# Kernel optimization log

Hardware: AMD Instinct MI355X
Metric: run time of the kernel (lower is better)

## Reference

```python
import jax, jax.numpy as jnp
import numpy as np

V = 65536      # vocab_size_v
H = 512        # hidden_size
M = 16         # max word length (m)
N = 8192       # number of words in the ragged batch
IH = H // 4    # char embedding dim / LSTM input size
HH = H // 2    # LSTM hidden size per direction


def setup_inputs() -> dict:
    key = jax.random.key(0)
    ks = jax.random.split(key, 16)
    word_ids = jax.random.randint(ks[0], (N,), 0, V, dtype=jnp.int32)
    is_oov = jax.random.randint(ks[1], (N,), 0, 2, dtype=jnp.int32)
    char_ids = jax.random.randint(ks[2], (N, M), 0, 256, dtype=jnp.int32)
    char_lens = jax.random.randint(ks[3], (N,), 1, M + 1, dtype=jnp.int32)
    lstm_scale = 1.0 / np.sqrt(HH)
    return {
        "word_ids": word_ids,
        "is_oov": is_oov,
        "char_ids": char_ids,
        "char_lens": char_lens,
        "word_emb": jax.random.normal(ks[4], (V, H), jnp.float32) * 0.02,
        "char_emb": jax.random.normal(ks[5], (256, IH), jnp.float32) * 0.02,
        "w_ih_f": jax.random.uniform(ks[6], (4 * HH, IH), jnp.float32, -lstm_scale, lstm_scale),
        "w_hh_f": jax.random.uniform(ks[7], (4 * HH, HH), jnp.float32, -lstm_scale, lstm_scale),
        "b_ih_f": jax.random.uniform(ks[8], (4 * HH,), jnp.float32, -lstm_scale, lstm_scale),
        "b_hh_f": jax.random.uniform(ks[9], (4 * HH,), jnp.float32, -lstm_scale, lstm_scale),
        "w_ih_b": jax.random.uniform(ks[10], (4 * HH, IH), jnp.float32, -lstm_scale, lstm_scale),
        "w_hh_b": jax.random.uniform(ks[11], (4 * HH, HH), jnp.float32, -lstm_scale, lstm_scale),
        "b_ih_b": jax.random.uniform(ks[12], (4 * HH,), jnp.float32, -lstm_scale, lstm_scale),
        "b_hh_b": jax.random.uniform(ks[13], (4 * HH,), jnp.float32, -lstm_scale, lstm_scale),
        "proj_w": jax.random.normal(ks[14], (H, H), jnp.float32) * 0.02,
        "proj_b": jax.random.normal(ks[15], (H,), jnp.float32) * 0.02,
    }


def _lstm_final_hidden(x, lens, w_ih, w_hh, b_ih, b_hh):
    """Batched variable-length LSTM; returns final hidden state h_T per sequence.

    x: [N, M, IH], lens: [N]. Carry is frozen once t >= len (emulating per-word
    batch-size-1 LSTM calls on unpadded sequences). PyTorch gate order i,f,g,o.
    """
    n = x.shape[0]
    gx = jnp.einsum("nmi,gi->nmg", x, w_ih) + b_ih + b_hh        # [N, M, 4HH]
    mask = (jnp.arange(M)[None, :] < lens[:, None])[..., None]    # [N, M, 1]

    def step(carry, inp):
        h, c = carry
        g_t, m_t = inp                                            # [N,4HH], [N,1]
        g = g_t + h @ w_hh.T
        i, f, gg, o = jnp.split(g, 4, axis=-1)
        i = jax.nn.sigmoid(i)
        f = jax.nn.sigmoid(f)
        gg = jnp.tanh(gg)
        o = jax.nn.sigmoid(o)
        c_new = f * c + i * gg
        h_new = o * jnp.tanh(c_new)
        h = jnp.where(m_t, h_new, h)
        c = jnp.where(m_t, c_new, c)
        return (h, c), None

    h0 = jnp.zeros((n, HH), x.dtype)
    c0 = jnp.zeros((n, HH), x.dtype)
    (h, _), _ = jax.lax.scan(step, (h0, c0),
                             (gx.transpose(1, 0, 2), mask.transpose(1, 0, 2)))
    return h  # [N, HH]


def reference(word_ids, is_oov, char_ids, char_lens,
              word_emb, char_emb,
              w_ih_f, w_hh_f, b_ih_f, b_hh_f,
              w_ih_b, w_hh_b, b_ih_b, b_hh_b,
              proj_w, proj_b):
    # Char-level path (computed for all words, selected only where OOV).
    x = char_emb[char_ids]                                        # [N, M, IH]
    h_fwd = _lstm_final_hidden(x, char_lens, w_ih_f, w_hh_f, b_ih_f, b_hh_f)
    # Backward direction: reverse each sequence within its true length.
    rev_idx = jnp.clip(char_lens[:, None] - 1 - jnp.arange(M)[None, :], 0, M - 1)
    x_rev = jnp.take_along_axis(x, rev_idx[..., None], axis=1)    # [N, M, IH]
    h_bwd = _lstm_final_hidden(x_rev, char_lens, w_ih_b, w_hh_b, b_ih_b, b_hh_b)
    char_word_embed = jnp.concatenate([h_fwd, h_bwd], axis=-1)    # [N, H]

    vocab_embed = word_emb[word_ids]                              # [N, H]
    sel = jnp.where(is_oov[:, None] > 0, char_word_embed, vocab_embed)
    return sel @ proj_w.T + proj_b                                # [N, H]
```

## Files before the change

kernel.cpp:

```cpp
#include <hip/hip_runtime.h>
#include <math.h>

#define VOCAB   65536
#define HDIM    512
#define MLEN    16
#define NWORDS  8192
#define IHDIM   128
#define HHDIM   256

#define TMW 32
#define TP  32

#define B_WHH 0u
#define B_GX2 1048576u
#define B_PBF 5242880u
#define B_PBB 5767168u
#define B_CHE 5769216u
#define B_INT 14157824u

typedef _Float16 f16x8 __attribute__((ext_vector_type(8)));
typedef float    f32x4 __attribute__((ext_vector_type(4)));
union U4H8 { uint4 u; f16x8 h; _Float16 e[8]; };

__device__ __forceinline__ unsigned packh2(float lo, float hi) {
    union { _Float16 h[2]; unsigned u; } v;
    v.h[0] = (_Float16)lo; v.h[1] = (_Float16)hi;
    return v.u;
}

__device__ __forceinline__ float sigf(float x)  { return 1.0f / (1.0f + __expf(-x)); }
__device__ __forceinline__ float tanh_f(float x){ return 1.0f - 2.0f / (__expf(2.0f * x) + 1.0f); }

__device__ __forceinline__ void load_lds_128(const void* g, void* l) {
    __builtin_amdgcn_global_load_lds((const __attribute__((address_space(1))) unsigned*)g,
                                     (__attribute__((address_space(3))) unsigned*)l, 16, 0, 0);
}

__global__ void prep_k(const float* __restrict__ whhf, const float* __restrict__ whhb,
                       const float* __restrict__ projw, const float* __restrict__ projb,
                       char* __restrict__ wsb) {
    int i = blockIdx.x * blockDim.x + threadIdx.x;
    if (i < 65536) {
        int dir = i >> 15, r = i & 32767, kt = r >> 12, r2 = r & 4095, ntg = r2 >> 6, lane = r2 & 63;
        const float* whh = dir ? whhb : whhf;
        int n  = ntg * 16 + (lane & 15);
        int k0 = kt * 32 + (lane >> 4) * 8;
        unsigned q[4];
        #pragma unroll
        for (int jj = 0; jj < 4; ++jj)
            q[jj] = packh2(whh[n * HHDIM + k0 + 2 * jj], whh[n * HHDIM + k0 + 2 * jj + 1]);
        ((uint4*)(wsb + B_WHH))[i] = make_uint4(q[0], q[1], q[2], q[3]);
    }
    if (i < 32768) {
        int kt = i >> 11, r = i & 2047, nt = r >> 6, lane = r & 63;
        int j  = nt * 16 + (lane & 15);
        int k0 = kt * 32 + (lane >> 4) * 8;
        unsigned q[4];
        #pragma unroll
        for (int jj = 0; jj < 4; ++jj)
            q[jj] = packh2(projw[j * HDIM + k0 + 2 * jj], projw[j * HDIM + k0 + 2 * jj + 1]);
        ((uint4*)(wsb + B_PBF))[i] = make_uint4(q[0], q[1], q[2], q[3]);
    }
    if (i < 512) ((float*)(wsb + B_PBB))[i] = projb[i];
}

__global__ void gxc_k(const float* __restrict__ wihf, const float* __restrict__ wihb,
                      const float* __restrict__ bihf, const float* __restrict__ bhhf,
                      const float* __restrict__ bihb, const float* __restrict__ bhhb,
                      const float* __restrict__ chemb, char* __restrict__ wsb) {
    const int dir = blockIdx.x >> 8, cid = blockIdx.x & 255;
    __shared__ __align__(16) float emb[IHDIM];
    __shared__ float gxl[1024];
    if (threadIdx.x < IHDIM) emb[threadIdx.x] = chemb[cid * IHDIM + threadIdx.x];
    __syncthreads();
    const float* wih = dir ? wihb : wihf;
    const float* bih = dir ? bihb : bihf;
    const float* bhh = dir ? bhhb : bhhf;
    #pragma unroll
    for (int p = 0; p < 4; ++p) {
        int n = threadIdx.x + p * 256;
        float acc = bih[n] + bhh[n];
        const float4* w4 = (const float4*)(wih + n * IHDIM);
        const float4* e4 = (const float4*)emb;
        #pragma unroll 8
        for (int k4 = 0; k4 < 32; ++k4) {
            float4 w = w4[k4], e = e4[k4];
            acc = fmaf(w.x, e.x, fmaf(w.y, e.y, fmaf(w.z, e.z, fmaf(w.w, e.w, acc))));
        }
        gxl[n] = acc;
    }
    __syncthreads();
    uint4* outp = (uint4*)(wsb + B_GX2) + (size_t)(dir * 256 + cid) * 512;
    #pragma unroll
    for (int s = 0; s < 2; ++s) {
        int tid2 = threadIdx.x + s * 256;
        int wv = tid2 >> 6, col = tid2 & 15;
        U4H8 v;
        #pragma unroll
        for (int g = 0; g < 4; ++g)
            #pragma unroll
            for (int c = 0; c < 2; ++c)
                v.e[g * 2 + c] = (_Float16)gxl[g * 256 + wv * 32 + c * 16 + col];
        outp[tid2] = v.u;
    }
}

__global__ void count_k(const int* __restrict__ is_oov, const int* __restrict__ lens,
                        int* __restrict__ ip) {
    int n = blockIdx.x * blockDim.x + threadIdx.x;
    if (n < NWORDS && is_oov[n] > 0) atomicAdd(&ip[lens[n] - 1], 1);
}

__global__ void prefix_k(int* __restrict__ ip) {
    if (threadIdx.x == 0) {
        int total = 0;
        for (int b = 15; b >= 0; --b) { ip[16 + b] = total; ip[32 + b] = total; total += ip[b]; }
        ip[48] = total;
    }
}

__global__ void scatter_k(const int* __restrict__ is_oov, const int* __restrict__ lens,
                          int* __restrict__ ip) {
    int n = blockIdx.x * blockDim.x + threadIdx.x;
    if (n < NWORDS && is_oov[n] > 0) {
        int pos = atomicAdd(&ip[32 + lens[n] - 1], 1);
        ip[64 + pos] = n;
    }
}

__global__ __launch_bounds__(512, 2)
void lstm_k(const int* __restrict__ char_ids, const int* __restrict__ lens,
            const char* __restrict__ wsb, const int* __restrict__ ip) {
    const int dir = blockIdx.y;
    const int tid = threadIdx.x;
    const int total = ip[48];
    const int w0 = blockIdx.x * TMW;
    if (w0 >= total) return;
    const int wcount = min(TMW, total - w0);
    const int* sorted = ip + 64;

    __shared__ int n_s[TMW], len_s[TMW];
    __shared__ int cid_s[MLEN][TMW];
    __shared__ __align__(16) _Float16 Zh[TMW][264];
    __shared__ __align__(16) uint4 wbuf[8][2][512];

    if (tid < TMW) {
        int idx = w0 + min(tid, wcount - 1);
        n_s[tid] = sorted[idx];
        len_s[tid] = (tid < wcount) ? lens[sorted[idx]] : 0;
    }
    for (int i = tid; i < TMW * 132; i += 512) ((unsigned*)Zh)[i] = 0u;
    __syncthreads();
    {
        int m = tid >> 4, t = tid & 15;
        int L = len_s[m];
        int pos = dir ? max(L - 1 - t, 0) : t;
        cid_s[t][m] = char_ids[n_s[m] * MLEN + pos];
    }

    const int wv = tid >> 6, lane = tid & 63, col = lane & 15, quad = lane >> 4;
    int lenr[2][4];
    #pragma unroll
    for (int mt = 0; mt < 2; ++mt)
        #pragma unroll
        for (int r = 0; r < 4; ++r) lenr[mt][r] = len_s[mt * 16 + quad * 4 + r];
    const int maxlen = len_s[0];

    const uint4* wpg = (const uint4*)(wsb + B_WHH) + (size_t)dir * 32768;
    const uint4* gx2 = (const uint4*)(wsb + B_GX2) + (size_t)dir * 131072;

    float cst[2][2][4];
    #pragma unroll
    for (int c = 0; c < 2; ++c)
        #pragma unroll
        for (int mt = 0; mt < 2; ++mt)
            #pragma unroll
            for (int r = 0; r < 4; ++r) cst[c][mt][r] = 0.0f;

    auto stage = [&](int kt, int buf) {
        #pragma unroll
        for (int gc = 0; gc < 8; ++gc) {
            int ntg = (gc >> 1) * 16 + wv * 2 + (gc & 1);
            load_lds_128(wpg + (kt * 4096 + ntg * 64 + lane), &wbuf[wv][buf][gc * 64]);
        }
    };
    stage(0, 0);
    __syncthreads();

    for (int t = 0; t < maxlen; ++t) {
        U4H8 gq[2][4];
        #pragma unroll
        for (int mt = 0; mt < 2; ++mt)
            #pragma unroll
            for (int r = 0; r < 4; ++r)
                gq[mt][r].u = gx2[(size_t)cid_s[t][mt * 16 + quad * 4 + r] * 512 + tid];

        f32x4 acc[4][2][2];
        #pragma unroll
        for (int g = 0; g < 4; ++g)
            #pragma unroll
            for (int c = 0; c < 2; ++c)
                #pragma unroll
                for (int mt = 0; mt < 2; ++mt) {
                    f32x4 a;
                    #pragma unroll
                    for (int r = 0; r < 4; ++r) a[r] = (float)gq[mt][r].e[g * 2 + c];
                    acc[g][c][mt] = a;
                }

        #pragma unroll
        for (int kt = 0; kt < 8; ++kt) {
            const int buf = kt & 1;
            stage((kt + 1) & 7, buf ^ 1);
            __builtin_amdgcn_s_waitcnt(0x0F78);
            f16x8 af0 = *(const f16x8*)&Zh[col][kt * 32 + quad * 8];
            f16x8 af1 = *(const f16x8*)&Zh[16 + col][kt * 32 + quad * 8];
            #pragma unroll
            for (int g = 0; g < 4; ++g)
                #pragma unroll
                for (int c = 0; c < 2; ++c) {
                    U4H8 b; b.u = wbuf[wv][buf][(g * 2 + c) * 64 + lane];
                    acc[g][c][0] = __builtin_amdgcn_mfma_f32_16x16x32_f16(af0, b.h, acc[g][c][0], 0, 0, 0);
                    acc[g][c][1] = __builtin_amdgcn_mfma_f32_16x16x32_f16(af1, b.h, acc[g][c][1], 0, 0, 0);
                }
        }
        __syncthreads();

        #pragma unroll
        for (int mt = 0; mt < 2; ++mt)
            #pragma unroll
            for (int r = 0; r < 4; ++r) {
                if (t < lenr[mt][r]) {
                    const int m = mt * 16 + quad * 4 + r;
                    #pragma unroll
                    for (int c = 0; c < 2; ++c) {
                        float i_ = sigf(acc[0][c][mt][r]);
                        float f_ = sigf(acc[1][c][mt][r]);
                        float g_ = tanh_f(acc[2][c][mt][r]);
                        float o_ = sigf(acc[3][c][mt][r]);
                        float cn = f_ * cst[c][mt][r] + i_ * g_;
                        cst[c][mt][r] = cn;
                        Zh[m][wv * 32 + c * 16 + col] = (_Float16)(o_ * tanh_f(cn));
                    }
                }
            }
        __syncthreads();
    }

    unsigned short* cheh = (unsigned short*)(wsb + B_CHE);
    for (int i = tid; i < TMW * HHDIM; i += 512) {
        int m = i >> 8, u = i & 255;
        if (m < wcount) {
            union { _Float16 h; unsigned short s; } v; v.h = Zh[m][u];
            __builtin_nontemporal_store(v.s, cheh + (size_t)n_s[m] * HDIM + dir * HHDIM + u);
        }
    }
}

__global__ __launch_bounds__(512, 2)
void proj_k(const int* __restrict__ word_ids, const int* __restrict__ is_oov,
            const float* __restrict__ word_emb, const char* __restrict__ wsb,
            float* __restrict__ out) {
    const int tid = threadIdx.x;
    const int n0 = blockIdx.x * TP;
    __shared__ __align__(16) _Float16 Zp[TP][520];

    for (int f = tid; f < TP * 128; f += 512) {
        int w = f >> 7, s4 = f & 127;
        int n = n0 + w;
        if (is_oov[n] > 0) {
            ushort4 hv = ((const ushort4*)((const unsigned short*)(wsb + B_CHE) + (size_t)n * HDIM))[s4];
            *(ushort4*)&Zp[w][s4 * 4] = hv;
        } else {
            float4 v = ((const float4*)(word_emb + (size_t)word_ids[n] * HDIM))[s4];
            Zp[w][s4 * 4 + 0] = (_Float16)v.x;
            Zp[w][s4 * 4 + 1] = (_Float16)v.y;
            Zp[w][s4 * 4 + 2] = (_Float16)v.z;
            Zp[w][s4 * 4 + 3] = (_Float16)v.w;
        }
    }
    __syncthreads();

    const int wv = tid >> 6, lane = tid & 63, col = lane & 15, quad = lane >> 4;
    const float* pbb = (const float*)(wsb + B_PBB);
    f32x4 acc[4][2];
    #pragma unroll
    for (int c = 0; c < 4; ++c) {
        float b = pbb[wv * 64 + c * 16 + col];
        acc[c][0] = (f32x4){b, b, b, b};
        acc[c][1] = (f32x4){b, b, b, b};
    }

    const uint4* pbf = (const uint4*)(wsb + B_PBF);
    #pragma unroll
    for (int kt = 0; kt < 16; ++kt) {
        f16x8 af0 = *(const f16x8*)&Zp[col][kt * 32 + quad * 8];
        f16x8 af1 = *(const f16x8*)&Zp[16 + col][kt * 32 + quad * 8];
        #pragma unroll
        for (int c = 0; c < 4; ++c) {
            U4H8 b; b.u = pbf[(size_t)kt * 2048 + (wv * 4 + c) * 64 + lane];
            acc[c][0] = __builtin_amdgcn_mfma_f32_16x16x32_f16(af0, b.h, acc[c][0], 0, 0, 0);
            acc[c][1] = __builtin_amdgcn_mfma_f32_16x16x32_f16(af1, b.h, acc[c][1], 0, 0, 0);
        }
    }

    #pragma unroll
    for (int mt = 0; mt < 2; ++mt)
        #pragma unroll
        for (int r = 0; r < 4; ++r) {
            const size_t m = n0 + mt * 16 + quad * 4 + r;
            #pragma unroll
            for (int c = 0; c < 4; ++c)
                __builtin_nontemporal_store(acc[c][mt][r], &out[m * HDIM + wv * 64 + c * 16 + col]);
        }
}

extern "C" void kernel_launch(void* const* d_in, const int* in_sizes, int n_in,
                              void* d_out, int out_size, void* d_ws, size_t ws_size,
                              hipStream_t stream) {
    const int*   word_ids  = (const int*)d_in[0];
    const int*   is_oov    = (const int*)d_in[1];
    const int*   char_ids  = (const int*)d_in[2];
    const int*   char_lens = (const int*)d_in[3];
    const float* word_emb  = (const float*)d_in[4];
    const float* char_emb  = (const float*)d_in[5];
    const float* w_ih_f    = (const float*)d_in[6];
    const float* w_hh_f    = (const float*)d_in[7];
    const float* b_ih_f    = (const float*)d_in[8];
    const float* b_hh_f    = (const float*)d_in[9];
    const float* w_ih_b    = (const float*)d_in[10];
    const float* w_hh_b    = (const float*)d_in[11];
    const float* b_ih_b    = (const float*)d_in[12];
    const float* b_hh_b    = (const float*)d_in[13];
    const float* proj_w    = (const float*)d_in[14];
    const float* proj_b    = (const float*)d_in[15];
    float* out = (float*)d_out;
    char*  wsb = (char*)d_ws;
    int*   ip  = (int*)(wsb + B_INT);

    hipMemsetAsync(ip, 0, 256, stream);
    prep_k<<<256, 256, 0, stream>>>(w_hh_f, w_hh_b, proj_w, proj_b, wsb);
    gxc_k<<<512, 256, 0, stream>>>(w_ih_f, w_ih_b, b_ih_f, b_hh_f, b_ih_b, b_hh_b, char_emb, wsb);
    count_k<<<NWORDS / 256, 256, 0, stream>>>(is_oov, char_lens, ip);
    prefix_k<<<1, 64, 0, stream>>>(ip);
    scatter_k<<<NWORDS / 256, 256, 0, stream>>>(is_oov, char_lens, ip);
    lstm_k<<<dim3(NWORDS / TMW, 2), 512, 0, stream>>>(char_ids, char_lens, wsb, ip);
    proj_k<<<NWORDS / TP, 512, 0, stream>>>(word_ids, is_oov, word_emb, wsb, out);
}
```

Baseline: 474.3 us.

## Keep part of W_hh in registers, restructure gx precompute, enlarge proj tile

The gate-input precompute is split into a kernel that stages W_ih rows in shared memory and writes an fp32 intermediate, plus a separate fp16 pack kernel. In the LSTM kernel, the first three k-tiles of W_hh are held in registers across all timesteps, so only the remaining tiles are streamed into LDS each step with a different waitcnt schedule. The LSTM grid is flattened so forward and backward blocks interleave, and the projection tile grows to 64 words per block for more reuse of the projection weights. These changes add register pressure, an extra launch and an extra intermediate buffer.

```diff
diff --git a/kernel.cpp b/kernel.cpp
--- a/kernel.cpp
+++ b/kernel.cpp
@@ -9,14 +9,15 @@
 #define HHDIM   256
 
 #define TMW 32
-#define TP  32
+#define TP  64
 
 #define B_WHH 0u
 #define B_GX2 1048576u
 #define B_PBF 5242880u
 #define B_PBB 5767168u
 #define B_CHE 5769216u
-#define B_INT 14157824u
+#define B_GXL 14157824u
+#define B_INT 16254976u
 
 typedef _Float16 f16x8 __attribute__((ext_vector_type(8)));
 typedef float    f32x4 __attribute__((ext_vector_type(4)));
@@ -64,45 +65,50 @@
     if (i < 512) ((float*)(wsb + B_PBB))[i] = projb[i];
 }
 
-__global__ void gxc_k(const float* __restrict__ wihf, const float* __restrict__ wihb,
+__global__ void gxa_k(const float* __restrict__ wihf, const float* __restrict__ wihb,
                       const float* __restrict__ bihf, const float* __restrict__ bhhf,
                       const float* __restrict__ bihb, const float* __restrict__ bhhb,
                       const float* __restrict__ chemb, char* __restrict__ wsb) {
-    const int dir = blockIdx.x >> 8, cid = blockIdx.x & 255;
-    __shared__ __align__(16) float emb[IHDIM];
-    __shared__ float gxl[1024];
-    if (threadIdx.x < IHDIM) emb[threadIdx.x] = chemb[cid * IHDIM + threadIdx.x];
-    __syncthreads();
+    const int dir = blockIdx.x >> 5, nc = blockIdx.x & 31, n0 = nc * 32;
+    __shared__ __align__(16) float swih[32 * IHDIM];
+    __shared__ float sb[32];
     const float* wih = dir ? wihb : wihf;
     const float* bih = dir ? bihb : bihf;
     const float* bhh = dir ? bhhb : bhhf;
-    #pragma unroll
-    for (int p = 0; p < 4; ++p) {
-        int n = threadIdx.x + p * 256;
-        float acc = bih[n] + bhh[n];
-        const float4* w4 = (const float4*)(wih + n * IHDIM);
-        const float4* e4 = (const float4*)emb;
-        #pragma unroll 8
+    for (int i = threadIdx.x; i < 1024; i += 256)
+        ((float4*)swih)[i] = ((const float4*)(wih + (size_t)n0 * IHDIM))[i];
+    if (threadIdx.x < 32) sb[threadIdx.x] = bih[n0 + threadIdx.x] + bhh[n0 + threadIdx.x];
+    __syncthreads();
+    const int cid = threadIdx.x;
+    float4 emb[32];
+    #pragma unroll
+    for (int k4 = 0; k4 < 32; ++k4) emb[k4] = ((const float4*)(chemb + cid * IHDIM))[k4];
+    float* gxl = (float*)(wsb + B_GXL) + (size_t)dir * 262144;
+    for (int n = 0; n < 32; ++n) {
+        float acc = sb[n];
+        const float4* w4 = (const float4*)(swih + n * IHDIM);
+        #pragma unroll
         for (int k4 = 0; k4 < 32; ++k4) {
-            float4 w = w4[k4], e = e4[k4];
+            float4 w = w4[k4], e = emb[k4];
             acc = fmaf(w.x, e.x, fmaf(w.y, e.y, fmaf(w.z, e.z, fmaf(w.w, e.w, acc))));
         }
-        gxl[n] = acc;
-    }
-    __syncthreads();
-    uint4* outp = (uint4*)(wsb + B_GX2) + (size_t)(dir * 256 + cid) * 512;
-    #pragma unroll
-    for (int s = 0; s < 2; ++s) {
-        int tid2 = threadIdx.x + s * 256;
-        int wv = tid2 >> 6, col = tid2 & 15;
-        U4H8 v;
-        #pragma unroll
-        for (int g = 0; g < 4; ++g)
-            #pragma unroll
-            for (int c = 0; c < 2; ++c)
-                v.e[g * 2 + c] = (_Float16)gxl[g * 256 + wv * 32 + c * 16 + col];
-        outp[tid2] = v.u;
-    }
+        gxl[(size_t)(n0 + n) * 256 + cid] = acc;
+    }
+}
+
+__global__ void pack_k(char* __restrict__ wsb) {
+    int i = blockIdx.x * blockDim.x + threadIdx.x;
+    int dir = i >> 17, r = i & 131071, cid = r >> 9, t2 = r & 511;
+    int wv = t2 >> 6, col = t2 & 15;
+    const float* gxl = (const float*)(wsb + B_GXL) + (size_t)dir * 262144;
+    U4H8 v;
+    #pragma unroll
+    for (int j = 0; j < 8; ++j) {
+        int g = j >> 1, c = j & 1;
+        int n = g * 256 + wv * 32 + c * 16 + col;
+        v.e[j] = (_Float16)gxl[(size_t)n * 256 + cid];
+    }
+    ((uint4*)(wsb + B_GX2))[i] = v.u;
 }
 
 __global__ void count_k(const int* __restrict__ is_oov, const int* __restrict__ lens,
@@ -131,10 +137,11 @@
 __global__ __launch_bounds__(512, 2)
 void lstm_k(const int* __restrict__ char_ids, const int* __restrict__ lens,
             const char* __restrict__ wsb, const int* __restrict__ ip) {
-    const int dir = blockIdx.y;
+    const int b = blockIdx.x;
+    const int dir = b & 1;
     const int tid = threadIdx.x;
     const int total = ip[48];
-    const int w0 = blockIdx.x * TMW;
+    const int w0 = (b >> 1) * TMW;
     if (w0 >= total) return;
     const int wcount = min(TMW, total - w0);
     const int* sorted = ip + 64;
@@ -169,6 +176,15 @@
     const uint4* wpg = (const uint4*)(wsb + B_WHH) + (size_t)dir * 32768;
     const uint4* gx2 = (const uint4*)(wsb + B_GX2) + (size_t)dir * 131072;
 
+    uint4 wreg[3][8];
+    #pragma unroll
+    for (int kt = 0; kt < 3; ++kt)
+        #pragma unroll
+        for (int gc = 0; gc < 8; ++gc) {
+            int ntg = (gc >> 1) * 16 + wv * 2 + (gc & 1);
+            wreg[kt][gc] = wpg[kt * 4096 + ntg * 64 + lane];
+        }
+
     float cst[2][2][4];
     #pragma unroll
     for (int c = 0; c < 2; ++c)
@@ -184,10 +200,10 @@
             load_lds_128(wpg + (kt * 4096 + ntg * 64 + lane), &wbuf[wv][buf][gc * 64]);
         }
     };
-    stage(0, 0);
     __syncthreads();
 
     for (int t = 0; t < maxlen; ++t) {
+        stage(3, 1);
         U4H8 gq[2][4];
         #pragma unroll
         for (int mt = 0; mt < 2; ++mt)
@@ -210,19 +226,23 @@
 
         #pragma unroll
         for (int kt = 0; kt < 8; ++kt) {
-            const int buf = kt & 1;
-            stage((kt + 1) & 7, buf ^ 1);
-            __builtin_amdgcn_s_waitcnt(0x0F78);
+            if (kt == 0) stage(4, 0);
+            if (kt >= 3 && kt < 7) __builtin_amdgcn_s_waitcnt(0x0F78);
+            if (kt == 7)           __builtin_amdgcn_s_waitcnt(0x0F70);
             f16x8 af0 = *(const f16x8*)&Zh[col][kt * 32 + quad * 8];
             f16x8 af1 = *(const f16x8*)&Zh[16 + col][kt * 32 + quad * 8];
             #pragma unroll
-            for (int g = 0; g < 4; ++g)
-                #pragma unroll
-                for (int c = 0; c < 2; ++c) {
-                    U4H8 b; b.u = wbuf[wv][buf][(g * 2 + c) * 64 + lane];
-                    acc[g][c][0] = __builtin_amdgcn_mfma_f32_16x16x32_f16(af0, b.h, acc[g][c][0], 0, 0, 0);
-                    acc[g][c][1] = __builtin_amdgcn_mfma_f32_16x16x32_f16(af1, b.h, acc[g][c][1], 0, 0, 0);
-                }
+            for (int gc = 0; gc < 8; ++gc) {
+                U4H8 bf;
+                if (kt < 3) bf.u = wreg[kt][gc];
+                else        bf.u = wbuf[wv][kt & 1][gc * 64 + lane];
+                const int g = gc >> 1, c = gc & 1;
+                acc[g][c][0] = __builtin_amdgcn_mfma_f32_16x16x32_f16(af0, bf.h, acc[g][c][0], 0, 0, 0);
+                acc[g][c][1] = __builtin_amdgcn_mfma_f32_16x16x32_f16(af1, bf.h, acc[g][c][1], 0, 0, 0);
+            }
+            if (kt == 3) stage(5, 1);
+            if (kt == 4) stage(6, 0);
+            if (kt == 5) stage(7, 1);
         }
         __syncthreads();
 
@@ -283,29 +303,32 @@
 
     const int wv = tid >> 6, lane = tid & 63, col = lane & 15, quad = lane >> 4;
     const float* pbb = (const float*)(wsb + B_PBB);
-    f32x4 acc[4][2];
+    f32x4 acc[4][4];
     #pragma unroll
     for (int c = 0; c < 4; ++c) {
-        float b = pbb[wv * 64 + c * 16 + col];
-        acc[c][0] = (f32x4){b, b, b, b};
-        acc[c][1] = (f32x4){b, b, b, b};
+        float bv = pbb[wv * 64 + c * 16 + col];
+        #pragma unroll
+        for (int mt = 0; mt < 4; ++mt) acc[c][mt] = (f32x4){bv, bv, bv, bv};
     }
 
     const uint4* pbf = (const uint4*)(wsb + B_PBF);
     #pragma unroll
     for (int kt = 0; kt < 16; ++kt) {
-        f16x8 af0 = *(const f16x8*)&Zp[col][kt * 32 + quad * 8];
-        f16x8 af1 = *(const f16x8*)&Zp[16 + col][kt * 32 + quad * 8];
+        f16x8 af[4];
+        #pragma unroll
+        for (int mt = 0; mt < 4; ++mt)
+            af[mt] = *(const f16x8*)&Zp[mt * 16 + col][kt * 32 + quad * 8];
         #pragma unroll
         for (int c = 0; c < 4; ++c) {
-            U4H8 b; b.u = pbf[(size_t)kt * 2048 + (wv * 4 + c) * 64 + lane];
-            acc[c][0] = __builtin_amdgcn_mfma_f32_16x16x32_f16(af0, b.h, acc[c][0], 0, 0, 0);
-            acc[c][1] = __builtin_amdgcn_mfma_f32_16x16x32_f16(af1, b.h, acc[c][1], 0, 0, 0);
-        }
-    }
-
-    #pragma unroll
-    for (int mt = 0; mt < 2; ++mt)
+            U4H8 bf; bf.u = pbf[(size_t)kt * 2048 + (wv * 4 + c) * 64 + lane];
+            #pragma unroll
+            for (int mt = 0; mt < 4; ++mt)
+                acc[c][mt] = __builtin_amdgcn_mfma_f32_16x16x32_f16(af[mt], bf.h, acc[c][mt], 0, 0, 0);
+        }
+    }
+
+    #pragma unroll
+    for (int mt = 0; mt < 4; ++mt)
         #pragma unroll
         for (int r = 0; r < 4; ++r) {
             const size_t m = n0 + mt * 16 + quad * 4 + r;
@@ -340,10 +363,11 @@
 
     hipMemsetAsync(ip, 0, 256, stream);
     prep_k<<<256, 256, 0, stream>>>(w_hh_f, w_hh_b, proj_w, proj_b, wsb);
-    gxc_k<<<512, 256, 0, stream>>>(w_ih_f, w_ih_b, b_ih_f, b_hh_f, b_ih_b, b_hh_b, char_emb, wsb);
+    gxa_k<<<64, 256, 0, stream>>>(w_ih_f, w_ih_b, b_ih_f, b_hh_f, b_ih_b, b_hh_b, char_emb, wsb);
+    pack_k<<<1024, 256, 0, stream>>>(wsb);
     count_k<<<NWORDS / 256, 256, 0, stream>>>(is_oov, char_lens, ip);
     prefix_k<<<1, 64, 0, stream>>>(ip);
     scatter_k<<<NWORDS / 256, 256, 0, stream>>>(is_oov, char_lens, ip);
-    lstm_k<<<dim3(NWORDS / TMW, 2), 512, 0, stream>>>(char_ids, char_lens, wsb, ip);
+    lstm_k<<<2 * (NWORDS / TMW), 512, 0, stream>>>(char_ids, char_lens, wsb, ip);
     proj_k<<<NWORDS / TP, 512, 0, stream>>>(word_ids, is_oov, word_emb, wsb, out);
 }
```

Measured after the change: 683.0 us. +44.0%, slower.
